# Kernel tuning notes

Hardware: AMD Instinct MI355X
Metric: run time of the kernel (lower is better)

Reference implementation:

```python
import jax, jax.numpy as jnp
import numpy as np

N_ATTR = 100000   # rows of ndata (node attribute table)
MAX_Z = 100000    # config['max_z']
ATTR_DIM = 64
HID = 32          # hidden_units
NUM_LAYERS = 3
K = 30            # SortPooling k
B = 1024          # number of graphs in the batch
NPG = 256         # nodes per graph
N = B * NPG       # 262144 total nodes
EPG = 4096        # edges per graph
E = B * EPG       # 4194304 total edges
D_LAT = HID * NUM_LAYERS + 1  # 97
DENSE_DIM = (((K - 2) // 2 + 1) - 5 + 1) * 32  # 352


def setup_inputs() -> dict:
    key = jax.random.key(0)
    ks = jax.random.split(key, 24)
    # edges confined within each subgraph (batched graph structure)
    offs = jnp.repeat(jnp.arange(B, dtype=jnp.int32) * NPG, EPG)
    src = offs + jax.random.randint(ks[0], (E,), 0, NPG, dtype=jnp.int32)
    dst = offs + jax.random.randint(ks[1], (E,), 0, NPG, dtype=jnp.int32)
    node_id = jax.random.randint(ks[2], (N,), 0, min(N_ATTR, MAX_Z))
    feats = jax.random.randint(ks[3], (N,), 0, 1000)  # structural z-labels
    edge_id = jax.random.randint(ks[4], (E,), 0, E)
    ndata = jax.random.normal(ks[5], (N_ATTR, ATTR_DIM), jnp.float32)
    edata = jax.random.uniform(ks[6], (E, 1), jnp.float32)
    node_emb = jax.random.normal(ks[7], (N_ATTR + MAX_Z, HID), jnp.float32) * 0.1
    s = 0.05
    d_in = ATTR_DIM + 2 * HID  # 128
    W0 = jax.random.normal(ks[8], (d_in, HID), jnp.float32) * s
    W1 = jax.random.normal(ks[9], (HID, HID), jnp.float32) * s
    W2 = jax.random.normal(ks[10], (HID, HID), jnp.float32) * s
    W3 = jax.random.normal(ks[11], (HID, 1), jnp.float32) * s
    b0 = jnp.zeros((HID,), jnp.float32)
    b1 = jnp.zeros((HID,), jnp.float32)
    b2 = jnp.zeros((HID,), jnp.float32)
    b3 = jnp.zeros((1,), jnp.float32)
    conv1_w = jax.random.normal(ks[12], (16, 1, D_LAT), jnp.float32) * s
    conv1_b = jnp.zeros((16,), jnp.float32)
    conv2_w = jax.random.normal(ks[13], (32, 16, 5), jnp.float32) * s
    conv2_b = jnp.zeros((32,), jnp.float32)
    fc1_w = jax.random.normal(ks[14], (128, DENSE_DIM), jnp.float32) * s
    fc1_b = jnp.zeros((128,), jnp.float32)
    fc2_w = jax.random.normal(ks[15], (1, 128), jnp.float32) * s
    fc2_b = jnp.zeros((1,), jnp.float32)
    return dict(feats=feats, node_id=node_id, edge_id=edge_id, src=src, dst=dst,
                ndata=ndata, edata=edata, node_emb=node_emb,
                W0=W0, b0=b0, W1=W1, b1=b1, W2=W2, b2=b2, W3=W3, b3=b3,
                conv1_w=conv1_w, conv1_b=conv1_b, conv2_w=conv2_w, conv2_b=conv2_b,
                fc1_w=fc1_w, fc1_b=fc1_b, fc2_w=fc2_w, fc2_b=fc2_b)


def _dgcnn_forward(feats, node_id, edge_id, src, dst, ndata, edata, node_emb,
                   W0, b0, W1, b1, W2, b2, W3, b3,
                   conv1_w, conv1_b, conv2_w, conv2_b, fc1_w, fc1_b, fc2_w, fc2_b):
    # --- input features: 3-way embedding concat ---
    x = jnp.concatenate([ndata[node_id], node_emb[feats],
                         node_emb[N_ATTR + node_id]], axis=1)  # [N, 128]
    ew = edata[edge_id][:, 0]  # [E] edge weights
    # DGL GraphConv norm='both': unweighted degree normalization, clamp(min=1)
    ones = jnp.ones((E,), jnp.float32)
    deg_out = jnp.clip(jax.ops.segment_sum(ones, src, num_segments=N), 1.0)
    deg_in = jnp.clip(jax.ops.segment_sum(ones, dst, num_segments=N), 1.0)
    ns = (deg_out ** -0.5)[:, None]  # src norm
    nd = (deg_in ** -0.5)[:, None]   # dst norm

    def gconv(h, W, b):
        # out = D_in^{-1/2} * scatter_add(dst, (D_out^{-1/2} h)[src] * ew) @ W + b
        m = (h * ns)[src] * ew[:, None]                       # [E, d]
        agg = jax.ops.segment_sum(m, dst, num_segments=N)     # [N, d]
        return jnp.tanh((agg * nd) @ W + b)

    h1 = gconv(x, W0, b0)    # [N, 32]
    h2 = gconv(h1, W1, b1)   # [N, 32]
    h3 = gconv(h2, W2, b2)   # [N, 32]
    h4 = gconv(h3, W3, b3)   # [N, 1]
    feat = jnp.concatenate([h1, h2, h3, h4], axis=-1)  # [N, 97]

    # --- SortPooling (DGL): sort each node's features ascending along feature
    # dim, then take top-K nodes per graph sorted descending by last feature ---
    fs = jnp.sort(feat, axis=-1).reshape(B, NPG, D_LAT)
    keys = fs[:, :, -1]                                  # [B, NPG]
    _, idx = jax.lax.top_k(keys, K)                      # [B, K]
    pooled = jnp.take_along_axis(fs, idx[:, :, None], axis=1)  # [B, K, 97]
    z = pooled.reshape(B, 1, K * D_LAT)                  # [B, 1, 2910]

    # --- CNN: Conv1d(1,16,97,stride 97) -> ReLU -> MaxPool(2,2) -> Conv1d(16,32,5) -> ReLU ---
    dn = ('NCH', 'OIH', 'NCH')
    z = jax.lax.conv_general_dilated(z, conv1_w, (D_LAT,), 'VALID', dimension_numbers=dn)
    z = jax.nn.relu(z + conv1_b[None, :, None])          # [B, 16, 30]
    z = jax.lax.reduce_window(z, -jnp.inf, jax.lax.max, (1, 1, 2), (1, 1, 2), 'VALID')  # [B,16,15]
    z = jax.lax.conv_general_dilated(z, conv2_w, (1,), 'VALID', dimension_numbers=dn)
    z = jax.nn.relu(z + conv2_b[None, :, None])          # [B, 32, 11]

    # --- MLP (dropout is identity in eval) ---
    z = z.reshape(B, -1)                                 # [B, 352]
    z = jax.nn.relu(z @ fc1_w.T + fc1_b)
    return z @ fc2_w.T + fc2_b                           # [B, 1]


def reference(feats, node_id, edge_id, src, dst, ndata, edata, node_emb,
              W0, b0, W1, b1, W2, b2, W3, b3,
              conv1_w, conv1_b, conv2_w, conv2_b, fc1_w, fc1_b, fc2_w, fc2_b):
    return _dgcnn_forward(feats, node_id, edge_id, src, dst, ndata, edata, node_emb,
                          W0, b0, W1, b1, W2, b2, W3, b3,
                          conv1_w, conv1_b, conv2_w, conv2_b, fc1_w, fc1_b, fc2_w, fc2_b)
```

## Files before the change

### kernel.cpp

```cpp
#include <hip/hip_runtime.h>
#include <math.h>

#define NPG    256
#define EPG    4096
#define NGRAPH 1024
#define NATTR  100000

__device__ float g_F[(size_t)NGRAPH * NPG * 100];
__device__ uint2 g_edges[(size_t)NGRAPH * EPG + 8];

#define A_BUFA   0
#define A_BUFB   36864
#define A_ROWS   73728
#define A_NS     74784
#define A_ND     75808
#define A_BS     76832
#define A_KEYS   77344
#define A_Y4     78368
#define A_SEL    79392
#define A_TOTAL  79520

#define E_DEGI   0
#define E_DEGO   1024
#define E_CUR    2048

#define H_S30    0
#define H_C1W    12000
#define H_C2W    18208
#define H_L1     28448
#define H_Q      30368
#define H_RR     31328
#define H_FF     32736

__device__ __forceinline__ void aggregate32(const uint2* __restrict__ gE,
                                            const int* rowS, const float* Y,
                                            const float* ns, const float* nd,
                                            const float* Bs, int boff,
                                            float* Hout, float* keys,
                                            float* __restrict__ gFg, int t)
{
    #pragma unroll
    for (int r = 0; r < 2; ++r) {
        const int n = r * 128 + (t >> 3);
        const int q = t & 7;
        const int rs = rowS[n], re = rowS[n + 1];
        double a0 = 0.0, a1 = 0.0, a2 = 0.0, a3 = 0.0;
        uint2 e0 = gE[rs];
        float4 y0 = *(const float4*)(Y + e0.y * 36 + q * 4);
        for (int e = rs; e < re; ++e) {
            const uint2 e1 = gE[e + 1];
            const float4 y1 = *(const float4*)(Y + e1.y * 36 + q * 4);
            const double w = (double)__uint_as_float(e0.x);
            a0 += (double)y0.x * w;
            a1 += (double)y0.y * w;
            a2 += (double)y0.z * w;
            a3 += (double)y0.w * w;
            e0 = e1; y0 = y1;
        }
        const double sc = (double)nd[n];
        float4 hv;
        hv.x = tanhf((float)(a0 * sc) + Bs[boff + q * 4 + 0]);
        hv.y = tanhf((float)(a1 * sc) + Bs[boff + q * 4 + 1]);
        hv.z = tanhf((float)(a2 * sc) + Bs[boff + q * 4 + 2]);
        hv.w = tanhf((float)(a3 * sc) + Bs[boff + q * 4 + 3]);
        *(float4*)(gFg + (size_t)n * 100 + boff + q * 4) = hv;
        const float s2 = ns[n];
        float4 o; o.x = hv.x * s2; o.y = hv.y * s2; o.z = hv.z * s2; o.w = hv.w * s2;
        *(float4*)(Hout + n * 36 + q * 4) = o;
        float m = fmaxf(fmaxf(hv.x, hv.y), fmaxf(hv.z, hv.w));
        m = fmaxf(m, __shfl_xor(m, 1, 64));
        m = fmaxf(m, __shfl_xor(m, 2, 64));
        m = fmaxf(m, __shfl_xor(m, 4, 64));
        if (q == 0) keys[n] = fmaxf(keys[n], m);
    }
}

extern "C" __global__ void __launch_bounds__(1024, 8)
dgcnn_fused(const int* __restrict__ feats, const int* __restrict__ node_id,
            const int* __restrict__ edge_id, const int* __restrict__ src,
            const int* __restrict__ dst,
            const float* __restrict__ ndata, const float* __restrict__ edata,
            const float* __restrict__ node_emb,
            const float* __restrict__ W0, const float* __restrict__ b0,
            const float* __restrict__ W1, const float* __restrict__ b1,
            const float* __restrict__ W2, const float* __restrict__ b2,
            const float* __restrict__ W3, const float* __restrict__ b3,
            const float* __restrict__ c1w, const float* __restrict__ c1b,
            const float* __restrict__ c2w, const float* __restrict__ c2b,
            const float* __restrict__ f1w, const float* __restrict__ f1b,
            const float* __restrict__ f2w, const float* __restrict__ f2b,
            float* __restrict__ out)
{
    extern __shared__ char smem[];
    float* BufA = (float*)(smem + A_BUFA);
    float* BufB = (float*)(smem + A_BUFB);
    int*   rowS = (int*)(smem + A_ROWS);
    float* ns   = (float*)(smem + A_NS);
    float* nd   = (float*)(smem + A_ND);
    float* Bs   = (float*)(smem + A_BS);
    float* keys = (float*)(smem + A_KEYS);
    float* y4   = (float*)(smem + A_Y4);
    int*   selI = (int*)(smem + A_SEL);

    const int g = blockIdx.x, t = threadIdx.x;
    const int lane = t & 63, wv = t >> 6;
    float* gFg = g_F + (size_t)g * NPG * 100;
    uint2* gE  = g_edges + (size_t)g * EPG;

    int* degI = (int*)((char*)BufA + E_DEGI);
    int* degO = (int*)((char*)BufA + E_DEGO);
    int* cur  = (int*)((char*)BufA + E_CUR);
    float* ewRaw = BufB;

    if (t < NPG) { degI[t] = 0; degO[t] = 0; keys[t] = -INFINITY; }
    if (t < 97) Bs[t] = (t < 32) ? b0[t] : (t < 64) ? b1[t - 32]
                       : (t < 96) ? b2[t - 64] : b3[0];
    __syncthreads();
    for (int e = t; e < EPG; e += 1024) {
        const int ge = g * EPG + e;
        const int s = src[ge] - g * NPG;
        const int d = dst[ge] - g * NPG;
        ewRaw[e] = edata[edge_id[ge]];
        atomicAdd(&degO[s], 1);
        atomicAdd(&degI[d], 1);
    }
    __syncthreads();
    if (t < 64) {
        const int d0 = degI[4 * t], d1 = degI[4 * t + 1],
                  d2 = degI[4 * t + 2], d3 = degI[4 * t + 3];
        const int p1 = d0, p2 = p1 + d1, p3 = p2 + d2, p4 = p3 + d3;
        int s = p4;
        #pragma unroll
        for (int off = 1; off <= 32; off <<= 1) {
            const int o = __shfl_up(s, off, 64);
            if (lane >= off) s += o;
        }
        const int excl = s - p4;
        rowS[4 * t + 1] = excl + p1;
        rowS[4 * t + 2] = excl + p2;
        rowS[4 * t + 3] = excl + p3;
        rowS[4 * t + 4] = excl + p4;
        if (t == 0) rowS[0] = 0;
    }
    __syncthreads();
    if (t < NPG) {
        ns[t] = (float)(1.0 / sqrt((double)(degO[t] > 0 ? degO[t] : 1)));
        nd[t] = (float)(1.0 / sqrt((double)(degI[t] > 0 ? degI[t] : 1)));
        cur[t] = rowS[t];
    }
    __syncthreads();
    for (int e = t; e < EPG; e += 1024) {
        const int ge = g * EPG + e;
        const int s = src[ge] - g * NPG;
        const int d = dst[ge] - g * NPG;
        const int pos = atomicAdd(&cur[d], 1);
        gE[pos] = make_uint2(__float_as_uint(ewRaw[e]), (uint)s);
    }
    __syncthreads();

    const int j = t & 31, nb = t >> 5;

    {
        float acc[8] = {0.f, 0.f, 0.f, 0.f, 0.f, 0.f, 0.f, 0.f};
        for (int c = 0; c < 4; ++c) {
            for (int i = t; i < 2048; i += 1024) {
                const int n = i >> 3, q = i & 7;
                const int gn = g * NPG + n;
                const int nidn = node_id[gn];
                const int j0 = c * 32 + q * 4;
                float4 v;
                if (j0 < 64)      v = *(const float4*)(ndata    + (size_t)nidn * 64 + j0);
                else if (j0 < 96) v = *(const float4*)(node_emb + (size_t)feats[gn] * 32 + (j0 - 64));
                else              v = *(const float4*)(node_emb + (size_t)(NATTR + nidn) * 32 + (j0 - 96));
                const float sc = ns[n];
                float4 o; o.x = v.x * sc; o.y = v.y * sc; o.z = v.z * sc; o.w = v.w * sc;
                *(float4*)(BufB + n * 36 + q * 4) = o;
            }
            __syncthreads();
            float wc[32];
            #pragma unroll
            for (int d = 0; d < 32; ++d) wc[d] = W0[(c * 32 + d) * 32 + j];
            #pragma unroll
            for (int i2 = 0; i2 < 8; ++i2) {
                const int n = nb * 8 + i2;
                const float4* ar = (const float4*)(BufB + n * 36);
                float a = acc[i2];
                #pragma unroll
                for (int d8 = 0; d8 < 8; ++d8) {
                    const float4 av = ar[d8];
                    a = fmaf(av.x, wc[4 * d8 + 0], a);
                    a = fmaf(av.y, wc[4 * d8 + 1], a);
                    a = fmaf(av.z, wc[4 * d8 + 2], a);
                    a = fmaf(av.w, wc[4 * d8 + 3], a);
                }
                acc[i2] = a;
            }
            __syncthreads();
        }
        #pragma unroll
        for (int i2 = 0; i2 < 8; ++i2) BufB[(nb * 8 + i2) * 36 + j] = acc[i2];
        __syncthreads();
        aggregate32(gE, rowS, BufB, ns, nd, Bs, 0, BufA, keys, gFg, t);
        __syncthreads();
    }

    for (int L = 0; L < 2; ++L) {
        const float* WL = L ? W2 : W1;
        float wc[32];
        #pragma unroll
        for (int d = 0; d < 32; ++d) wc[d] = WL[d * 32 + j];
        float acc[8];
        #pragma unroll
        for (int i2 = 0; i2 < 8; ++i2) {
            const int n = nb * 8 + i2;
            const float4* fr = (const float4*)(BufA + n * 36);
            float a = 0.f;
            #pragma unroll
            for (int d8 = 0; d8 < 8; ++d8) {
                const float4 av = fr[d8];
                a = fmaf(av.x, wc[4 * d8 + 0], a);
                a = fmaf(av.y, wc[4 * d8 + 1], a);
                a = fmaf(av.z, wc[4 * d8 + 2], a);
                a = fmaf(av.w, wc[4 * d8 + 3], a);
            }
            acc[i2] = a;
        }
        __syncthreads();
        #pragma unroll
        for (int i2 = 0; i2 < 8; ++i2) BufB[(nb * 8 + i2) * 36 + j] = acc[i2];
        __syncthreads();
        aggregate32(gE, rowS, BufB, ns, nd, Bs, 32 + L * 32, BufA, keys, gFg, t);
        __syncthreads();
    }

    if (t < NPG) {
        const float4* fr = (const float4*)(BufA + t * 36);
        float a = 0.f;
        #pragma unroll
        for (int d8 = 0; d8 < 8; ++d8) {
            const float4 h = fr[d8];
            a = fmaf(h.x, W3[4 * d8 + 0], a);
            a = fmaf(h.y, W3[4 * d8 + 1], a);
            a = fmaf(h.z, W3[4 * d8 + 2], a);
            a = fmaf(h.w, W3[4 * d8 + 3], a);
        }
        y4[t] = a;
    }
    __syncthreads();
    {
        const int n = t >> 2, p = t & 3;
        const int rs = rowS[n], re = rowS[n + 1];
        double a = 0.0;
        for (int e = rs + p; e < re; e += 4) {
            const uint2 ed = gE[e];
            a += (double)__uint_as_float(ed.x) * (double)y4[ed.y];
        }
        a += __shfl_xor(a, 1, 64);
        a += __shfl_xor(a, 2, 64);
        if (p == 0) {
            const float h = tanhf((float)(a * (double)nd[n]) + Bs[96]);
            gFg[(size_t)n * 100 + 96] = h;
            keys[n] = fmaxf(keys[n], h);
        }
    }
    __syncthreads();

    char*  HB   = (char*)BufA;
    float* S30  = (float*)(HB + H_S30);
    float* c1wS = (float*)(HB + H_C1W);
    float* c2wS = (float*)(HB + H_C2W);
    float* L1   = (float*)(HB + H_L1);
    float* Q    = (float*)(HB + H_Q);
    float* Rr   = (float*)(HB + H_RR);
    float* Ff   = (float*)(HB + H_FF);

    if (t < 64) {
        float kv[4]; int ki[4];
        #pragma unroll
        for (int r = 0; r < 4; ++r) { ki[r] = lane * 4 + r; kv[r] = keys[lane * 4 + r]; }
        for (int it = 0; it < 30; ++it) {
            float bv = kv[0]; int bi = ki[0];
            #pragma unroll
            for (int r = 1; r < 4; ++r)
                if (kv[r] > bv || (kv[r] == bv && ki[r] < bi)) { bv = kv[r]; bi = ki[r]; }
            #pragma unroll
            for (int off = 1; off <= 32; off <<= 1) {
                const float ov = __shfl_xor(bv, off, 64);
                const int   oi = __shfl_xor(bi, off, 64);
                if (ov > bv || (ov == bv && oi < bi)) { bv = ov; bi = oi; }
            }
            if (lane == 0) selI[it] = bi;
            if ((bi >> 2) == lane) kv[bi & 3] = -INFINITY;
        }
    } else {
        for (int i = t - 64; i < 1552; i += 960) c1wS[i] = c1w[i];
        for (int i = t - 64; i < 2560; i += 960) c2wS[i] = c2w[i];
    }
    __syncthreads();

    for (int k = wv; k < 30; k += 16) {
        const float* fr = gFg + (size_t)selI[k] * 100;
        float v0 = fr[lane];
        float v1 = (lane < 33) ? fr[64 + lane] : INFINITY;
        for (int kk = 2; kk <= 128; kk <<= 1) {
            for (int jj = kk >> 1; jj > 0; jj >>= 1) {
                if (jj == 64) {
                    const float lo = fminf(v0, v1), hi = fmaxf(v0, v1);
                    v0 = lo; v1 = hi;
                } else {
                    const float p0 = __shfl_xor(v0, jj, 64);
                    const float p1 = __shfl_xor(v1, jj, 64);
                    const bool up   = ((lane & jj) == 0);
                    const bool asc0 = (kk == 128) ? true : ((lane & kk) == 0);
                    const bool asc1 = (kk == 128) ? true : (((64 + lane) & kk) == 0);
                    v0 = (up == asc0) ? fminf(v0, p0) : fmaxf(v0, p0);
                    v1 = (up == asc1) ? fminf(v1, p1) : fmaxf(v1, p1);
                }
            }
        }
        S30[k * 100 + lane] = v0;
        if (lane < 33) S30[k * 100 + 64 + lane] = v1;
    }
    __syncthreads();

    if (t < 480) {
        const int k = t >> 4, c = t & 15;
        const float* row  = S30 + k * 100;
        const float* wrow = c1wS + c * 97;
        float acc = c1b[c];
        for (int d = 0; d < 97; ++d) acc = fmaf(row[d], wrow[d], acc);
        L1[k * 16 + c] = fmaxf(acc, 0.f);
    }
    __syncthreads();
    if (t < 240) {
        const int c = t / 15, tt = t % 15;
        Q[c * 15 + tt] = fmaxf(L1[(2 * tt) * 16 + c], L1[(2 * tt + 1) * 16 + c]);
    }
    __syncthreads();
    if (t < 352) {
        const int o = t / 11, tt = t % 11;
        const float* wo = c2wS + o * 80;
        float acc = c2b[o];
        #pragma unroll
        for (int c = 0; c < 16; ++c)
            #pragma unroll
            for (int jj = 0; jj < 5; ++jj)
                acc = fmaf(Q[c * 15 + tt + jj], wo[c * 5 + jj], acc);
        Rr[o * 11 + tt] = fmaxf(acc, 0.f);
    }
    __syncthreads();
    if (t < 128) {
        float acc = f1b[t];
        const float* wr = f1w + t * 352;
        for (int i = 0; i < 352; ++i) acc = fmaf(Rr[i], wr[i], acc);
        Ff[t] = fmaxf(acc, 0.f);
    }
    __syncthreads();
    if (t < 64) {
        float acc = Ff[lane] * f2w[lane] + Ff[lane + 64] * f2w[lane + 64];
        #pragma unroll
        for (int off = 1; off <= 32; off <<= 1) acc += __shfl_xor(acc, off, 64);
        if (lane == 0) out[g] = acc + f2b[0];
    }
}

extern "C" void kernel_launch(void* const* d_in, const int* in_sizes, int n_in,
                              void* d_out, int out_size, void* d_ws, size_t ws_size,
                              hipStream_t stream)
{
    const int*   feats    = (const int*)d_in[0];
    const int*   node_id  = (const int*)d_in[1];
    const int*   edge_id  = (const int*)d_in[2];
    const int*   src      = (const int*)d_in[3];
    const int*   dst      = (const int*)d_in[4];
    const float* ndata    = (const float*)d_in[5];
    const float* edata    = (const float*)d_in[6];
    const float* node_emb = (const float*)d_in[7];
    const float* W0 = (const float*)d_in[8];
    const float* b0 = (const float*)d_in[9];
    const float* W1 = (const float*)d_in[10];
    const float* b1 = (const float*)d_in[11];
    const float* W2 = (const float*)d_in[12];
    const float* b2 = (const float*)d_in[13];
    const float* W3 = (const float*)d_in[14];
    const float* b3 = (const float*)d_in[15];
    const float* c1w = (const float*)d_in[16];
    const float* c1b = (const float*)d_in[17];
    const float* c2w = (const float*)d_in[18];
    const float* c2b = (const float*)d_in[19];
    const float* f1w = (const float*)d_in[20];
    const float* f1b = (const float*)d_in[21];
    const float* f2w = (const float*)d_in[22];
    const float* f2b = (const float*)d_in[23];

    (void)hipFuncSetAttribute((const void*)dgcnn_fused,
                              hipFuncAttributeMaxDynamicSharedMemorySize, A_TOTAL);

    dgcnn_fused<<<NGRAPH, 1024, A_TOTAL, stream>>>(feats, node_id, edge_id, src, dst,
                                                   ndata, edata, node_emb,
                                                   W0, b0, W1, b1, W2, b2, W3, b3,
                                                   c1w, c1b, c2w, c2b,
                                                   f1w, f1b, f2w, f2b,
                                                   (float*)d_out);
}
```

Baseline: 390.2 us.

## Keep CSR edges in LDS, sort nodes by degree, drop global edge buffer

Builds the per-graph CSR edge list in shared memory instead of a global scratch buffer, caching packed src/dst in LDS so the second edge pass does not reread global memory. It adds a counting sort of nodes by in-degree so that threads in a wavefront aggregate nodes of similar degree, which reduces divergence. It also removes the second LDS feature buffer by reading the previous layer's outputs back from the global g_F and applying the ns scaling after the matmul. This frees LDS for the edges, but adds global re-reads of layer features and extra setup syncs.

New measurement: 370.0 us. -5.2%, faster.

```diff
diff --git a/kernel.cpp b/kernel.cpp
--- a/kernel.cpp
+++ b/kernel.cpp
@@ -7,22 +7,24 @@
 #define NATTR  100000
 
 __device__ float g_F[(size_t)NGRAPH * NPG * 100];
-__device__ uint2 g_edges[(size_t)NGRAPH * EPG + 8];
-
-#define A_BUFA   0
-#define A_BUFB   36864
-#define A_ROWS   73728
-#define A_NS     74784
-#define A_ND     75808
-#define A_BS     76832
-#define A_KEYS   77344
-#define A_Y4     78368
-#define A_SEL    79392
-#define A_TOTAL  79520
-
-#define E_DEGI   0
-#define E_DEGO   1024
-#define E_CUR    2048
+
+#define A_Y      0
+#define A_E      36864
+#define A_ROWS   69696
+#define A_NS     70752
+#define A_ND     71776
+#define A_BS     72800
+#define A_KEYS   73312
+#define A_Y4     74336
+#define A_SEL    75360
+#define A_ORD    75488
+#define A_TOTAL  76000
+
+#define E_EWRAW  0
+#define E_RAWSD  16384
+#define E_DEGI   32768
+#define E_DEGO   33792
+#define E_CUR    34816
 
 #define H_S30    0
 #define H_C1W    12000
@@ -32,30 +34,29 @@
 #define H_RR     31328
 #define H_FF     32736
 
-__device__ __forceinline__ void aggregate32(const uint2* __restrict__ gE,
-                                            const int* rowS, const float* Y,
-                                            const float* ns, const float* nd,
-                                            const float* Bs, int boff,
-                                            float* Hout, float* keys,
-                                            float* __restrict__ gFg, int t)
+__device__ __forceinline__ void aggregate32(const uint2* sE, const int* rowS,
+                                            const ushort* ord, const float* Y,
+                                            const float* nd, const float* Bs, int boff,
+                                            float* keys, float* __restrict__ gFg, int t)
 {
     #pragma unroll
     for (int r = 0; r < 2; ++r) {
-        const int n = r * 128 + (t >> 3);
+        const int n = ord[r * 128 + (t >> 3)];
         const int q = t & 7;
         const int rs = rowS[n], re = rowS[n + 1];
         double a0 = 0.0, a1 = 0.0, a2 = 0.0, a3 = 0.0;
-        uint2 e0 = gE[rs];
+        uint2 e0 = sE[rs];
+        uint2 e1 = sE[rs + 1];
         float4 y0 = *(const float4*)(Y + e0.y * 36 + q * 4);
         for (int e = rs; e < re; ++e) {
-            const uint2 e1 = gE[e + 1];
             const float4 y1 = *(const float4*)(Y + e1.y * 36 + q * 4);
+            const uint2 e2 = sE[e + 2];
             const double w = (double)__uint_as_float(e0.x);
             a0 += (double)y0.x * w;
             a1 += (double)y0.y * w;
             a2 += (double)y0.z * w;
             a3 += (double)y0.w * w;
-            e0 = e1; y0 = y1;
+            e0 = e1; e1 = e2; y0 = y1;
         }
         const double sc = (double)nd[n];
         float4 hv;
@@ -64,9 +65,6 @@
         hv.z = tanhf((float)(a2 * sc) + Bs[boff + q * 4 + 2]);
         hv.w = tanhf((float)(a3 * sc) + Bs[boff + q * 4 + 3]);
         *(float4*)(gFg + (size_t)n * 100 + boff + q * 4) = hv;
-        const float s2 = ns[n];
-        float4 o; o.x = hv.x * s2; o.y = hv.y * s2; o.z = hv.z * s2; o.w = hv.w * s2;
-        *(float4*)(Hout + n * 36 + q * 4) = o;
         float m = fmaxf(fmaxf(hv.x, hv.y), fmaxf(hv.z, hv.w));
         m = fmaxf(m, __shfl_xor(m, 1, 64));
         m = fmaxf(m, __shfl_xor(m, 2, 64));
@@ -92,34 +90,37 @@
             float* __restrict__ out)
 {
     extern __shared__ char smem[];
-    float* BufA = (float*)(smem + A_BUFA);
-    float* BufB = (float*)(smem + A_BUFB);
-    int*   rowS = (int*)(smem + A_ROWS);
-    float* ns   = (float*)(smem + A_NS);
-    float* nd   = (float*)(smem + A_ND);
-    float* Bs   = (float*)(smem + A_BS);
-    float* keys = (float*)(smem + A_KEYS);
-    float* y4   = (float*)(smem + A_Y4);
-    int*   selI = (int*)(smem + A_SEL);
+    float*  Y    = (float*)(smem + A_Y);
+    uint2*  sE   = (uint2*)(smem + A_E);
+    int*    rowS = (int*)(smem + A_ROWS);
+    float*  ns   = (float*)(smem + A_NS);
+    float*  nd   = (float*)(smem + A_ND);
+    float*  Bs   = (float*)(smem + A_BS);
+    float*  keys = (float*)(smem + A_KEYS);
+    float*  y4   = (float*)(smem + A_Y4);
+    int*    selI = (int*)(smem + A_SEL);
+    ushort* ord  = (ushort*)(smem + A_ORD);
 
     const int g = blockIdx.x, t = threadIdx.x;
     const int lane = t & 63, wv = t >> 6;
     float* gFg = g_F + (size_t)g * NPG * 100;
-    uint2* gE  = g_edges + (size_t)g * EPG;
-
-    int* degI = (int*)((char*)BufA + E_DEGI);
-    int* degO = (int*)((char*)BufA + E_DEGO);
-    int* cur  = (int*)((char*)BufA + E_CUR);
-    float* ewRaw = BufB;
+
+    float* ewRaw = (float*)((char*)Y + E_EWRAW);
+    uint*  rawSD = (uint*)((char*)Y + E_RAWSD);
+    int*   degI  = (int*)((char*)Y + E_DEGI);
+    int*   degO  = (int*)((char*)Y + E_DEGO);
+    int*   cur   = (int*)((char*)Y + E_CUR);
 
     if (t < NPG) { degI[t] = 0; degO[t] = 0; keys[t] = -INFINITY; }
     if (t < 97) Bs[t] = (t < 32) ? b0[t] : (t < 64) ? b1[t - 32]
                        : (t < 96) ? b2[t - 64] : b3[0];
+    if (t < 4) sE[4096 + t] = make_uint2(0u, 0u);
     __syncthreads();
     for (int e = t; e < EPG; e += 1024) {
         const int ge = g * EPG + e;
         const int s = src[ge] - g * NPG;
         const int d = dst[ge] - g * NPG;
+        rawSD[e] = (uint)s | ((uint)d << 16);
         ewRaw[e] = edata[edge_id[ge]];
         atomicAdd(&degO[s], 1);
         atomicAdd(&degI[d], 1);
@@ -150,11 +151,36 @@
     }
     __syncthreads();
     for (int e = t; e < EPG; e += 1024) {
-        const int ge = g * EPG + e;
-        const int s = src[ge] - g * NPG;
-        const int d = dst[ge] - g * NPG;
+        const uint sd = rawSD[e];
+        const int d = (int)(sd >> 16), s = (int)(sd & 0xffffu);
         const int pos = atomicAdd(&cur[d], 1);
-        gE[pos] = make_uint2(__float_as_uint(ewRaw[e]), (uint)s);
+        sE[pos] = make_uint2(__float_as_uint(ewRaw[e]), (uint)s);
+    }
+    __syncthreads();
+    if (t < NPG) degO[t] = 0;
+    __syncthreads();
+    if (t < NPG) atomicAdd(&degO[min(degI[t], 255)], 1);
+    __syncthreads();
+    if (t < 64) {
+        const int d0 = degO[4 * t], d1 = degO[4 * t + 1],
+                  d2 = degO[4 * t + 2], d3 = degO[4 * t + 3];
+        const int p1 = d0, p2 = p1 + d1, p3 = p2 + d2, p4 = p3 + d3;
+        int s = p4;
+        #pragma unroll
+        for (int off = 1; off <= 32; off <<= 1) {
+            const int o = __shfl_up(s, off, 64);
+            if (lane >= off) s += o;
+        }
+        const int excl = s - p4;
+        cur[4 * t]     = excl;
+        cur[4 * t + 1] = excl + p1;
+        cur[4 * t + 2] = excl + p2;
+        cur[4 * t + 3] = excl + p3;
+    }
+    __syncthreads();
+    if (t < NPG) {
+        const int pos = atomicAdd(&cur[min(degI[t], 255)], 1);
+        ord[pos] = (ushort)t;
     }
     __syncthreads();
 
@@ -174,7 +200,7 @@
                 else              v = *(const float4*)(node_emb + (size_t)(NATTR + nidn) * 32 + (j0 - 96));
                 const float sc = ns[n];
                 float4 o; o.x = v.x * sc; o.y = v.y * sc; o.z = v.z * sc; o.w = v.w * sc;
-                *(float4*)(BufB + n * 36 + q * 4) = o;
+                *(float4*)(Y + n * 36 + q * 4) = o;
             }
             __syncthreads();
             float wc[32];
@@ -183,7 +209,7 @@
             #pragma unroll
             for (int i2 = 0; i2 < 8; ++i2) {
                 const int n = nb * 8 + i2;
-                const float4* ar = (const float4*)(BufB + n * 36);
+                const float4* ar = (const float4*)(Y + n * 36);
                 float a = acc[i2];
                 #pragma unroll
                 for (int d8 = 0; d8 < 8; ++d8) {
@@ -198,14 +224,15 @@
             __syncthreads();
         }
         #pragma unroll
-        for (int i2 = 0; i2 < 8; ++i2) BufB[(nb * 8 + i2) * 36 + j] = acc[i2];
+        for (int i2 = 0; i2 < 8; ++i2) Y[(nb * 8 + i2) * 36 + j] = acc[i2];
         __syncthreads();
-        aggregate32(gE, rowS, BufB, ns, nd, Bs, 0, BufA, keys, gFg, t);
+        aggregate32(sE, rowS, ord, Y, nd, Bs, 0, keys, gFg, t);
         __syncthreads();
     }
 
     for (int L = 0; L < 2; ++L) {
         const float* WL = L ? W2 : W1;
+        const int pb = L ? 32 : 0;
         float wc[32];
         #pragma unroll
         for (int d = 0; d < 32; ++d) wc[d] = WL[d * 32 + j];
@@ -213,7 +240,7 @@
         #pragma unroll
         for (int i2 = 0; i2 < 8; ++i2) {
             const int n = nb * 8 + i2;
-            const float4* fr = (const float4*)(BufA + n * 36);
+            const float4* fr = (const float4*)(gFg + (size_t)n * 100 + pb);
             float a = 0.f;
             #pragma unroll
             for (int d8 = 0; d8 < 8; ++d8) {
@@ -223,18 +250,18 @@
                 a = fmaf(av.z, wc[4 * d8 + 2], a);
                 a = fmaf(av.w, wc[4 * d8 + 3], a);
             }
-            acc[i2] = a;
+            acc[i2] = a * ns[n];
         }
         __syncthreads();
         #pragma unroll
-        for (int i2 = 0; i2 < 8; ++i2) BufB[(nb * 8 + i2) * 36 + j] = acc[i2];
+        for (int i2 = 0; i2 < 8; ++i2) Y[(nb * 8 + i2) * 36 + j] = acc[i2];
         __syncthreads();
-        aggregate32(gE, rowS, BufB, ns, nd, Bs, 32 + L * 32, BufA, keys, gFg, t);
+        aggregate32(sE, rowS, ord, Y, nd, Bs, 32 + L * 32, keys, gFg, t);
         __syncthreads();
     }
 
     if (t < NPG) {
-        const float4* fr = (const float4*)(BufA + t * 36);
+        const float4* fr = (const float4*)(gFg + (size_t)t * 100 + 64);
         float a = 0.f;
         #pragma unroll
         for (int d8 = 0; d8 < 8; ++d8) {
@@ -244,15 +271,15 @@
             a = fmaf(h.z, W3[4 * d8 + 2], a);
             a = fmaf(h.w, W3[4 * d8 + 3], a);
         }
-        y4[t] = a;
+        y4[t] = a * ns[t];
     }
     __syncthreads();
     {
-        const int n = t >> 2, p = t & 3;
+        const int n = ord[t >> 2], p = t & 3;
         const int rs = rowS[n], re = rowS[n + 1];
         double a = 0.0;
         for (int e = rs + p; e < re; e += 4) {
-            const uint2 ed = gE[e];
+            const uint2 ed = sE[e];
             a += (double)__uint_as_float(ed.x) * (double)y4[ed.y];
         }
         a += __shfl_xor(a, 1, 64);
@@ -265,7 +292,7 @@
     }
     __syncthreads();
 
-    char*  HB   = (char*)BufA;
+    char*  HB   = (char*)Y;
     float* S30  = (float*)(HB + H_S30);
     float* c1wS = (float*)(HB + H_C1W);
     float* c2wS = (float*)(HB + H_C2W);
```
